# Kernel tuning notes

Hardware: AMD Instinct MI355X
Metric: run time of the kernel (lower is better)

Reference implementation:

```python
import jax, jax.numpy as jnp
import numpy as np

N_NODES = 50000
N_EDGES = 800000
FEAT_IN = 128
POS_IN = 16
EDGE_FEAT_IN = 16
H = 64
L = 4


def _lin(k, fan_in, fan_out):
    kw, kb = jax.random.split(k)
    s = 1.0 / np.sqrt(fan_in)
    W = jax.random.uniform(kw, (fan_in, fan_out), minval=-s, maxval=s, dtype=jnp.float32)
    b = jax.random.uniform(kb, (fan_out,), minval=-s, maxval=s, dtype=jnp.float32)
    return W, b


def setup_inputs() -> dict:
    key = jax.random.key(0)
    ks = jax.random.split(key, 32)
    h = jax.random.normal(ks[0], (N_NODES, FEAT_IN), dtype=jnp.float32)
    e = jax.random.normal(ks[1], (N_EDGES, EDGE_FEAT_IN), dtype=jnp.float32)
    p = jax.random.normal(ks[2], (N_NODES, POS_IN), dtype=jnp.float32)
    edge_index = jax.random.randint(ks[3], (2, N_EDGES), 0, N_NODES, dtype=jnp.int64 if jax.config.x64_enabled else jnp.int32)
    he_W, he_b = _lin(ks[4], FEAT_IN, H)
    ee_W, ee_b = _lin(ks[5], EDGE_FEAT_IN, H)
    pe_W, pe_b = _lin(ks[6], POS_IN, H)

    def stack(fan_in, base):
        Ws, bs = [], []
        for i in range(L):
            W, b = _lin(jax.random.fold_in(ks[7], base * 100 + i), fan_in, H)
            Ws.append(W); bs.append(b)
        return jnp.stack(Ws), jnp.stack(bs)

    hm_W, hm_b = stack(5 * H, 0)  # h_message_mlp
    hu_W, hu_b = stack(2 * H, 1)  # h_update
    eu_W, eu_b = stack(3 * H, 2)  # e_update
    pm_W, pm_b = stack(3 * H, 3)  # p_message_mlp
    pu_W, pu_b = stack(2 * H, 4)  # p_update
    return dict(h=h, e=e, p=p, edge_index=edge_index,
                he_W=he_W, he_b=he_b, ee_W=ee_W, ee_b=ee_b, pe_W=pe_W, pe_b=pe_b,
                hm_W=hm_W, hm_b=hm_b, hu_W=hu_W, hu_b=hu_b,
                eu_W=eu_W, eu_b=eu_b, pm_W=pm_W, pm_b=pm_b, pu_W=pu_W, pu_b=pu_b)


def reference(h, e, p, edge_index, he_W, he_b, ee_W, ee_b, pe_W, pe_b,
              hm_W, hm_b, hu_W, hu_b, eu_W, eu_b, pm_W, pm_b, pu_W, pu_b):
    send, rec = edge_index[0], edge_index[1]
    n = h.shape[0]
    h = h @ he_W + he_b  # [N,H]
    e = e @ ee_W + ee_b  # [E,H]
    p = p @ pe_W + pe_b  # [N,H]
    for i in range(L):
        hp_send = jnp.concatenate((h[send], p[send]), axis=1)  # [E,2H]
        hp_rec = jnp.concatenate((h[rec], p[rec]), axis=1)     # [E,2H]
        h_msg = jnp.concatenate((hp_send, hp_rec, e), axis=1) @ hm_W[i] + hm_b[i]  # [E,H]
        h_agg = jax.ops.segment_sum(h_msg, rec, num_segments=n)  # [N,H]
        h = jnp.concatenate((h, h_agg), axis=1) @ hu_W[i] + hu_b[i]
        e = jnp.concatenate((h[send], h[rec], e), axis=1) @ eu_W[i] + eu_b[i]
        p_msg = jnp.concatenate((p[send], p[rec], e), axis=1) @ pm_W[i] + pm_b[i]
        p_agg = jax.ops.segment_sum(p_msg, rec, num_segments=n)
        p = jnp.concatenate((p, p_agg), axis=1) @ pu_W[i] + pu_b[i]
    return (h, p)
```

## Files before the change

### kernel.cpp

```cpp
#include <hip/hip_runtime.h>
#include <hip/hip_bf16.h>

#define NN 50000
#define NE 800000

typedef __hip_bfloat16 bf16;
typedef __attribute__((ext_vector_type(8))) short bf16x8s;
typedef __attribute__((ext_vector_type(4))) float f32x4;

#define OFF_HP     0L
#define OFF_HSUM   12800000L
#define OFF_PSUM   25600000L
#define OFF_ESUM   38400000L
#define OFF_EAGGA  41600000L
#define OFF_EAGGB  54400000L
#define OFF_WFMT   67200000L
#define OFF_ROWPTR 67716096L
#define OFF_COLIDX 67916100L
#define OFF_SSEND  71116100L
#define OFF_SEG    74316100L
#define OFF_CNT    77516100L
#define OFF_BSUM   77716100L

#define SCAN_B 196

#define FW_HE 0
#define FW_EE 8192
#define FW_PE 10240
#define FW_L0 12288
#define LSTR  61440
#define R_HAGG 0
#define R_HMR  12288
#define R_HU   20480
#define R_EUS  28672
#define R_EUR  32768
#define R_EUE  36864
#define R_PAGG 40960
#define R_PMR  49152
#define R_PU   53248

#define AGG_STRIDE 72

__device__ __forceinline__ bf16x8s bfrag(const bf16* w, int c, int t, int lane) {
    return *(const bf16x8s*)(w + ((long)(c*4 + t)*64 + lane)*8);
}
__device__ __forceinline__ bf16x8s cvt8(const float* fp) {
    float4 f0 = ((const float4*)fp)[0];
    float4 f1 = ((const float4*)fp)[1];
    bf16 tmp[8];
    tmp[0]=__float2bfloat16(f0.x); tmp[1]=__float2bfloat16(f0.y);
    tmp[2]=__float2bfloat16(f0.z); tmp[3]=__float2bfloat16(f0.w);
    tmp[4]=__float2bfloat16(f1.x); tmp[5]=__float2bfloat16(f1.y);
    tmp[6]=__float2bfloat16(f1.z); tmp[7]=__float2bfloat16(f1.w);
    return *(const bf16x8s*)tmp;
}

__global__ __launch_bounds__(256) void wfmt_k(
    const float* __restrict__ he, const float* __restrict__ ee, const float* __restrict__ pe,
    const float* __restrict__ hm, const float* __restrict__ hu, const float* __restrict__ eu,
    const float* __restrict__ pm, const float* __restrict__ pu, bf16* __restrict__ wf)
{
    int s = blockIdx.x;
    const float* src = nullptr; int rowoff = 0, Ksrc = 0, Kpad = 0, mode = 0, split = 0, gap = 0; long doff = 0;
    if      (s == 0) { src = he; Ksrc = 128; Kpad = 128; doff = FW_HE; }
    else if (s == 1) { src = ee; Ksrc = 16;  Kpad = 32;  doff = FW_EE; }
    else if (s == 2) { src = pe; Ksrc = 16;  Kpad = 32;  doff = FW_PE; }
    else {
        int i = (s - 3) / 9, g = (s - 3) % 9;
        long base = FW_L0 + (long)i*LSTR;
        const float* HM = hm + (long)i*320*64;
        const float* HU = hu + (long)i*128*64;
        const float* EU = eu + (long)i*192*64;
        const float* PM = pm + (long)i*192*64;
        const float* PU = pu + (long)i*128*64;
        switch (g) {
          case 0:  src=HM; mode=4; split=128; gap=128; Kpad=192; doff=base+R_HAGG; break;
          case 1:  src=HM; rowoff=128; Ksrc=128; Kpad=128; doff=base+R_HMR;  break;
          case 2:  src=HU; rowoff=0;   Ksrc=128; Kpad=128; doff=base+R_HU;   break;
          case 3:  src=EU; rowoff=0;   Ksrc=64;  Kpad=64;  doff=base+R_EUS;  break;
          case 4:  src=EU; rowoff=64;  Ksrc=64;  Kpad=64;  doff=base+R_EUR;  break;
          case 5:  src=EU; rowoff=128; Ksrc=64;  Kpad=64;  doff=base+R_EUE;  break;
          case 6:  src=PM; mode=4; split=64; gap=64; Kpad=128; doff=base+R_PAGG; break;
          case 7:  src=PM; rowoff=64;  Ksrc=64;  Kpad=64;  doff=base+R_PMR;  break;
          default: src=PU; rowoff=0;   Ksrc=128; Kpad=128; doff=base+R_PU;   break;
        }
    }
    int total = Kpad * 64;
    for (int idx = threadIdx.x; idx < total; idx += 256) {
        int j = idx & 7, l = (idx >> 3) & 63, ct = idx >> 9;
        int c = ct >> 2, t = ct & 3;
        int k = c*32 + (l >> 4)*8 + j;
        int n = t*16 + (l & 15);
        float v;
        if (mode == 4) v = src[(long)(k + (k >= split ? gap : 0))*64 + n];
        else           v = (k < Ksrc) ? src[(long)(rowoff + k)*64 + n] : 0.f;
        wf[doff + idx] = __float2bfloat16(v);
    }
}

__global__ __launch_bounds__(256) void hist_k(const int* __restrict__ rec, int* __restrict__ cnt)
{
    int e = blockIdx.x*256 + threadIdx.x;
    if (e < NE) atomicAdd(&cnt[rec[e]], 1);
}

__global__ __launch_bounds__(256) void scan1_k(const int* __restrict__ cnt, int* __restrict__ bsum)
{
    __shared__ int sdata[256];
    int tid = threadIdx.x;
    int i = blockIdx.x*256 + tid;
    sdata[tid] = (i < NN) ? cnt[i] : 0;
    __syncthreads();
    #pragma unroll
    for (int off = 128; off > 0; off >>= 1) {
        if (tid < off) sdata[tid] += sdata[tid + off];
        __syncthreads();
    }
    if (tid == 0) bsum[blockIdx.x] = sdata[0];
}

__global__ __launch_bounds__(256) void scan2_k(int* __restrict__ bsum)
{
    __shared__ int sdata[256];
    int tid = threadIdx.x;
    int v = (tid < SCAN_B) ? bsum[tid] : 0;
    sdata[tid] = v;
    __syncthreads();
    #pragma unroll
    for (int off = 1; off < 256; off <<= 1) {
        int t = (tid >= off) ? sdata[tid - off] : 0;
        __syncthreads();
        sdata[tid] += t;
        __syncthreads();
    }
    if (tid < SCAN_B) bsum[tid] = sdata[tid] - v;
}

__global__ __launch_bounds__(256) void scan3_k(const int* __restrict__ cnt,
    const int* __restrict__ bsum, int* __restrict__ rowptr)
{
    __shared__ int sdata[256];
    int tid = threadIdx.x;
    int i = blockIdx.x*256 + tid;
    sdata[tid] = (i < NN) ? cnt[i] : 0;
    __syncthreads();
    #pragma unroll
    for (int off = 1; off < 256; off <<= 1) {
        int t = (tid >= off) ? sdata[tid - off] : 0;
        __syncthreads();
        sdata[tid] += t;
        __syncthreads();
    }
    if (i < NN) rowptr[i + 1] = sdata[tid] + bsum[blockIdx.x];
    if (i == 0) rowptr[0] = 0;
}

__global__ __launch_bounds__(256) void scatter_k(const int* __restrict__ rec,
    const int* __restrict__ rowptr, int* __restrict__ cursor, int* __restrict__ colidx)
{
    int e = blockIdx.x*256 + threadIdx.x;
    if (e < NE) {
        int r = rec[e];
        int pos = atomicAdd(&cursor[r], 1);
        colidx[rowptr[r] + pos] = e;
    }
}

__global__ __launch_bounds__(256) void segfill_k(const int* __restrict__ rowptr, int* __restrict__ seg)
{
    int n = blockIdx.x*256 + threadIdx.x;
    if (n < NN) {
        int b = rowptr[n], e = rowptr[n + 1];
        for (int j = b; j < e; ++j) seg[j] = n;
    }
}

template <int DEPTH, bool BOTH>
__global__ __launch_bounds__(256) void gsum64_k(const bf16* __restrict__ hp, int coff,
    const int* __restrict__ ssend, const int* __restrict__ seg,
    float* __restrict__ out1, float* __restrict__ out2)
{
    __shared__ int s_ids[256];
    __shared__ int s_seg[256];
    int tid = threadIdx.x, lane = tid & 63, wv = tid >> 6;
    int gbase = blockIdx.x*256;
    s_ids[tid] = ssend[gbase + tid];
    s_seg[tid] = seg[gbase + tid];
    __syncthreads();
    int j0 = wv*64;
    const bf16* base = hp + coff + lane;
    constexpr int NB = 64 / DEPTH;

    unsigned short va[DEPTH], vb[DEPTH];
    unsigned short wa[BOTH ? DEPTH : 1], wb[BOTH ? DEPTH : 1];
    #pragma unroll
    for (int k = 0; k < DEPTH; ++k) {
        long o = (long)s_ids[j0 + k]*128;
        va[k] = *(const unsigned short*)(base + o);
        if (BOTH) wa[k] = *(const unsigned short*)(base + o + 64);
    }

    float a = 0.f, b2 = 0.f;
    int cur = s_seg[j0];
    #pragma unroll
    for (int b = 0; b < NB; ++b) {
        if (b < NB - 1) {
            #pragma unroll
            for (int k = 0; k < DEPTH; ++k) {
                long o = (long)s_ids[j0 + (b+1)*DEPTH + k]*128;
                vb[k] = *(const unsigned short*)(base + o);
                if (BOTH) wb[k] = *(const unsigned short*)(base + o + 64);
            }
        }
        #pragma unroll
        for (int k = 0; k < DEPTH; ++k) {
            int n = s_seg[j0 + b*DEPTH + k];
            if (n != cur) {
                atomicAdd(&out1[(long)cur*64 + lane], a);
                if (BOTH) atomicAdd(&out2[(long)cur*64 + lane], b2);
                a = 0.f; b2 = 0.f; cur = n;
            }
            a += __uint_as_float(((unsigned)va[k]) << 16);
            if (BOTH) b2 += __uint_as_float(((unsigned)wa[k]) << 16);
        }
        if (b < NB - 1) {
            #pragma unroll
            for (int k = 0; k < DEPTH; ++k) { va[k] = vb[k]; if (BOTH) wa[k] = wb[k]; }
        }
    }
    atomicAdd(&out1[(long)cur*64 + lane], a);
    if (BOTH) atomicAdd(&out2[(long)cur*64 + lane], b2);
}

__global__ __launch_bounds__(256) void esum_k(const float* __restrict__ e_in,
    const int* __restrict__ colidx, const int* __restrict__ seg, const int* __restrict__ send,
    int* __restrict__ ssend, float* __restrict__ esum)
{
    __shared__ int s_ids[256];
    __shared__ int s_seg[256];
    int tid = threadIdx.x;
    int gbase = blockIdx.x*256;
    int id = colidx[gbase + tid];
    s_ids[tid] = id;
    s_seg[tid] = seg[gbase + tid];
    ssend[gbase + tid] = send[id];
    __syncthreads();
    int grp = tid >> 4, c = tid & 15;
    int j0 = grp*16;
    float vv[16];
    #pragma unroll
    for (int jj = 0; jj < 16; ++jj) vv[jj] = e_in[(long)s_ids[j0 + jj]*16 + c];
    float a = 0.f;
    int cur = s_seg[j0];
    #pragma unroll
    for (int jj = 0; jj < 16; ++jj) {
        int n = s_seg[j0 + jj];
        if (n != cur) { atomicAdd(&esum[(long)cur*16 + c], a); a = 0.f; cur = n; }
        a += vv[jj];
    }
    atomicAdd(&esum[(long)cur*16 + c], a);
}

__global__ __launch_bounds__(256) void eembn_k(const float* __restrict__ esum,
    const int* __restrict__ deg, const bf16* __restrict__ wEE, const float* __restrict__ ee_b,
    bf16* __restrict__ eagg)
{
    int tid = threadIdx.x, lane = tid & 63, wv = tid >> 6;
    int l15 = lane & 15, q = lane >> 4;
    int row = blockIdx.x*64 + wv*16 + l15;
    int rc = (row < NN) ? row : NN - 1;
    f32x4 acc[4];
    #pragma unroll
    for (int t = 0; t < 4; ++t) { acc[t][0]=0; acc[t][1]=0; acc[t][2]=0; acc[t][3]=0; }
    {
        bf16x8s af = {0,0,0,0,0,0,0,0};
        if (q < 2) af = cvt8(esum + (long)rc*16 + q*8);
        #pragma unroll
        for (int t = 0; t < 4; ++t)
            acc[t] = __builtin_amdgcn_mfma_f32_16x16x32_bf16(af, bfrag(wEE, 0, t, lane), acc[t], 0, 0, 0);
    }
    float bv[4];
    #pragma unroll
    for (int t = 0; t < 4; ++t) bv[t] = ee_b[t*16 + l15];
    #pragma unroll
    for (int r = 0; r < 4; ++r) {
        int ro = blockIdx.x*64 + wv*16 + q*4 + r;
        if (ro < NN) {
            float dg = (float)deg[ro];
            #pragma unroll
            for (int t = 0; t < 4; ++t)
                eagg[(long)ro*64 + t*16 + l15] = __float2bfloat16(acc[t][r] + dg*bv[t]);
        }
    }
}

__global__ __launch_bounds__(256) void hpemb_k(const float* __restrict__ h_in,
    const float* __restrict__ p_in,
    const bf16* __restrict__ wHE, const bf16* __restrict__ wPE,
    const float* __restrict__ he_b, const float* __restrict__ pe_b, bf16* __restrict__ hp)
{
    int tid = threadIdx.x, lane = tid & 63, wv = tid >> 6;
    int l15 = lane & 15, q = lane >> 4;
    int row = blockIdx.x*64 + wv*16 + l15;
    int rc = (row < NN) ? row : NN - 1;
    f32x4 aH[4], aP[4];
    #pragma unroll
    for (int t = 0; t < 4; ++t) {
        float bh = he_b[t*16 + l15], bp = pe_b[t*16 + l15];
        aH[t][0]=bh; aH[t][1]=bh; aH[t][2]=bh; aH[t][3]=bh;
        aP[t][0]=bp; aP[t][1]=bp; aP[t][2]=bp; aP[t][3]=bp;
    }
    #pragma unroll
    for (int c = 0; c < 4; ++c) {
        bf16x8s af = cvt8(h_in + (long)rc*128 + c*32 + q*8);
        #pragma unroll
        for (int t = 0; t < 4; ++t)
            aH[t] = __builtin_amdgcn_mfma_f32_16x16x32_bf16(af, bfrag(wHE, c, t, lane), aH[t], 0, 0, 0);
    }
    {
        bf16x8s af = {0,0,0,0,0,0,0,0};
        if (q < 2) af = cvt8(p_in + (long)rc*16 + q*8);
        #pragma unroll
        for (int t = 0; t < 4; ++t)
            aP[t] = __builtin_amdgcn_mfma_f32_16x16x32_bf16(af, bfrag(wPE, 0, t, lane), aP[t], 0, 0, 0);
    }
    #pragma unroll
    for (int r = 0; r < 4; ++r) {
        int ro = blockIdx.x*64 + wv*16 + q*4 + r;
        if (ro < NN)
            #pragma unroll
            for (int t = 0; t < 4; ++t) {
                hp[(long)ro*128 + t*16 + l15]      = __float2bfloat16(aH[t][r]);
                hp[(long)ro*128 + 64 + t*16 + l15] = __float2bfloat16(aP[t][r]);
            }
    }
}

__global__ __launch_bounds__(256) void hfuse_k(
    bf16* __restrict__ hp, float* __restrict__ hsum, const float* __restrict__ psum,
    const bf16* __restrict__ eagg, const int* __restrict__ deg,
    const bf16* __restrict__ wAGG, const bf16* __restrict__ wR, const float* __restrict__ mb,
    const bf16* __restrict__ wU, const float* __restrict__ ub, float* __restrict__ out2)
{
    __shared__ __align__(16) bf16 sAgg[64 * AGG_STRIDE];
    int tid = threadIdx.x, lane = tid & 63, wv = tid >> 6;
    int l15 = lane & 15, q = lane >> 4;
    int row = blockIdx.x*64 + wv*16 + l15;
    int rc = (row < NN) ? row : NN - 1;

    f32x4 aA[4], aR[4];
    #pragma unroll
    for (int t = 0; t < 4; ++t) {
        aA[t][0]=0;aA[t][1]=0;aA[t][2]=0;aA[t][3]=0;
        aR[t][0]=0;aR[t][1]=0;aR[t][2]=0;aR[t][3]=0;
    }
    #pragma unroll
    for (int c = 0; c < 6; ++c) {
        bf16x8s af = (c < 2) ? cvt8(hsum + (long)rc*64 + c*32 + q*8)
                   : (c < 4) ? cvt8(psum + (long)rc*64 + (c-2)*32 + q*8)
                             : *(const bf16x8s*)(eagg + (long)rc*64 + (c-4)*32 + q*8);
        #pragma unroll
        for (int t = 0; t < 4; ++t)
            aA[t] = __builtin_amdgcn_mfma_f32_16x16x32_bf16(af, bfrag(wAGG, c, t, lane), aA[t], 0, 0, 0);
    }
    if (row < NN) {
        float4 z4 = make_float4(0.f, 0.f, 0.f, 0.f);
        #pragma unroll
        for (int c = 0; c < 2; ++c) {
            *(float4*)(hsum + (long)rc*64 + c*32 + q*8)     = z4;
            *(float4*)(hsum + (long)rc*64 + c*32 + q*8 + 4) = z4;
        }
    }
    #pragma unroll
    for (int c = 0; c < 4; ++c) {
        bf16x8s af = *(const bf16x8s*)(hp + (long)rc*128 + c*32 + q*8);
        #pragma unroll
        for (int t = 0; t < 4; ++t)
            aR[t] = __builtin_amdgcn_mfma_f32_16x16x32_bf16(af, bfrag(wR, c, t, lane), aR[t], 0, 0, 0);
    }
    float mbv[4];
    #pragma unroll
    for (int t = 0; t < 4; ++t) mbv[t] = mb[t*16 + l15];
    #pragma unroll
    for (int r = 0; r < 4; ++r) {
        int ro = blockIdx.x*64 + wv*16 + q*4 + r;
        float dg = (float)deg[(ro < NN) ? ro : NN - 1];
        #pragma unroll
        for (int t = 0; t < 4; ++t)
            sAgg[(wv*16 + q*4 + r)*AGG_STRIDE + t*16 + l15] =
                __float2bfloat16(aA[t][r] + dg*(aR[t][r] + mbv[t]));
    }
    __syncthreads();
    f32x4 acc[4];
    #pragma unroll
    for (int t = 0; t < 4; ++t) { float b = ub[t*16 + l15]; acc[t][0]=b; acc[t][1]=b; acc[t][2]=b; acc[t][3]=b; }
    #pragma unroll
    for (int c = 0; c < 4; ++c) {
        bf16x8s af = (c < 2) ? *(const bf16x8s*)(hp + (long)rc*128 + c*32 + q*8)
                             : *(const bf16x8s*)(sAgg + (wv*16 + l15)*AGG_STRIDE + (c-2)*32 + q*8);
        #pragma unroll
        for (int t = 0; t < 4; ++t)
            acc[t] = __builtin_amdgcn_mfma_f32_16x16x32_bf16(af, bfrag(wU, c, t, lane), acc[t], 0, 0, 0);
    }
    #pragma unroll
    for (int r = 0; r < 4; ++r) {
        int ro = blockIdx.x*64 + wv*16 + q*4 + r;
        if (ro < NN) {
            #pragma unroll
            for (int t = 0; t < 4; ++t) {
                float fv = acc[t][r];
                hp[(long)ro*128 + t*16 + l15] = __float2bfloat16(fv);
                if (out2) out2[(long)ro*64 + t*16 + l15] = fv;
            }
        }
    }
}

__global__ __launch_bounds__(256) void pfuse_k(
    bf16* __restrict__ hp, const float* __restrict__ hsumN, float* __restrict__ psum,
    const bf16* __restrict__ eaggIn, bf16* __restrict__ eaggOut, const int* __restrict__ deg,
    const bf16* __restrict__ wEUS, const bf16* __restrict__ wEUR, const bf16* __restrict__ wEUE,
    const float* __restrict__ eub,
    const bf16* __restrict__ wAGG, const bf16* __restrict__ wR, const float* __restrict__ mb,
    const bf16* __restrict__ wU, const float* __restrict__ ub, float* __restrict__ out2)
{
    __shared__ __align__(16) bf16 sE[64 * AGG_STRIDE];
    __shared__ __align__(16) bf16 sAgg[64 * AGG_STRIDE];
    int tid = threadIdx.x, lane = tid & 63, wv = tid >> 6;
    int l15 = lane & 15, q = lane >> 4;
    int row = blockIdx.x*64 + wv*16 + l15;
    int rc = (row < NN) ? row : NN - 1;

    f32x4 aE[4], aH[4];
    #pragma unroll
    for (int t = 0; t < 4; ++t) {
        aE[t][0]=0;aE[t][1]=0;aE[t][2]=0;aE[t][3]=0;
        aH[t][0]=0;aH[t][1]=0;aH[t][2]=0;aH[t][3]=0;
    }
    #pragma unroll
    for (int c = 0; c < 4; ++c) {
        bf16x8s af = (c < 2) ? cvt8(hsumN + (long)rc*64 + c*32 + q*8)
                             : *(const bf16x8s*)(eaggIn + (long)rc*64 + (c-2)*32 + q*8);
        #pragma unroll
        for (int t = 0; t < 4; ++t) {
            bf16x8s w = (c < 2) ? bfrag(wEUS, c, t, lane) : bfrag(wEUE, c-2, t, lane);
            aE[t] = __builtin_amdgcn_mfma_f32_16x16x32_bf16(af, w, aE[t], 0, 0, 0);
        }
    }
    #pragma unroll
    for (int c = 0; c < 2; ++c) {
        bf16x8s af = *(const bf16x8s*)(hp + (long)rc*128 + c*32 + q*8);
        #pragma unroll
        for (int t = 0; t < 4; ++t)
            aH[t] = __builtin_amdgcn_mfma_f32_16x16x32_bf16(af, bfrag(wEUR, c, t, lane), aH[t], 0, 0, 0);
    }
    float ebv[4];
    #pragma unroll
    for (int t = 0; t < 4; ++t) ebv[t] = eub[t*16 + l15];
    #pragma unroll
    for (int r = 0; r < 4; ++r) {
        int ro = blockIdx.x*64 + wv*16 + q*4 + r;
        float dg = (float)deg[(ro < NN) ? ro : NN - 1];
        #pragma unroll
        for (int t = 0; t < 4; ++t) {
            bf16 ev = __float2bfloat16(aE[t][r] + dg*(aH[t][r] + ebv[t]));
            sE[(wv*16 + q*4 + r)*AGG_STRIDE + t*16 + l15] = ev;
            if (eaggOut && ro < NN) eaggOut[(long)ro*64 + t*16 + l15] = ev;
        }
    }
    __syncthreads();

    f32x4 aA[4], aR[4];
    #pragma unroll
    for (int t = 0; t < 4; ++t) {
        aA[t][0]=0;aA[t][1]=0;aA[t][2]=0;aA[t][3]=0;
        aR[t][0]=0;aR[t][1]=0;aR[t][2]=0;aR[t][3]=0;
    }
    #pragma unroll
    for (int c = 0; c < 4; ++c) {
        bf16x8s af = (c < 2) ? cvt8(psum + (long)rc*64 + c*32 + q*8)
                             : *(const bf16x8s*)(sE + (wv*16 + l15)*AGG_STRIDE + (c-2)*32 + q*8);
        #pragma unroll
        for (int t = 0; t < 4; ++t)
            aA[t] = __builtin_amdgcn_mfma_f32_16x16x32_bf16(af, bfrag(wAGG, c, t, lane), aA[t], 0, 0, 0);
    }
    if (row < NN) {
        float4 z4 = make_float4(0.f, 0.f, 0.f, 0.f);
        #pragma unroll
        for (int c = 0; c < 2; ++c) {
            *(float4*)(psum + (long)rc*64 + c*32 + q*8)     = z4;
            *(float4*)(psum + (long)rc*64 + c*32 + q*8 + 4) = z4;
        }
    }
    #pragma unroll
    for (int c = 0; c < 2; ++c) {
        bf16x8s af = *(const bf16x8s*)(hp + (long)rc*128 + 64 + c*32 + q*8);
        #pragma unroll
        for (int t = 0; t < 4; ++t)
            aR[t] = __builtin_amdgcn_mfma_f32_16x16x32_bf16(af, bfrag(wR, c, t, lane), aR[t], 0, 0, 0);
    }
    float mbv[4];
    #pragma unroll
    for (int t = 0; t < 4; ++t) mbv[t] = mb[t*16 + l15];
    #pragma unroll
    for (int r = 0; r < 4; ++r) {
        int ro = blockIdx.x*64 + wv*16 + q*4 + r;
        float dg = (float)deg[(ro < NN) ? ro : NN - 1];
        #pragma unroll
        for (int t = 0; t < 4; ++t)
            sAgg[(wv*16 + q*4 + r)*AGG_STRIDE + t*16 + l15] =
                __float2bfloat16(aA[t][r] + dg*(aR[t][r] + mbv[t]));
    }
    __syncthreads();
    f32x4 acc[4];
    #pragma unroll
    for (int t = 0; t < 4; ++t) { float b = ub[t*16 + l15]; acc[t][0]=b; acc[t][1]=b; acc[t][2]=b; acc[t][3]=b; }
    #pragma unroll
    for (int c = 0; c < 4; ++c) {
        bf16x8s af = (c < 2) ? *(const bf16x8s*)(hp + (long)rc*128 + 64 + c*32 + q*8)
                             : *(const bf16x8s*)(sAgg + (wv*16 + l15)*AGG_STRIDE + (c-2)*32 + q*8);
        #pragma unroll
        for (int t = 0; t < 4; ++t)
            acc[t] = __builtin_amdgcn_mfma_f32_16x16x32_bf16(af, bfrag(wU, c, t, lane), acc[t], 0, 0, 0);
    }
    #pragma unroll
    for (int r = 0; r < 4; ++r) {
        int ro = blockIdx.x*64 + wv*16 + q*4 + r;
        if (ro < NN) {
            #pragma unroll
            for (int t = 0; t < 4; ++t) {
                float fv = acc[t][r];
                hp[(long)ro*128 + 64 + t*16 + l15] = __float2bfloat16(fv);
                if (out2) out2[(long)ro*64 + t*16 + l15] = fv;
            }
        }
    }
}

extern "C" void kernel_launch(void* const* d_in, const int* in_sizes, int n_in,
                              void* d_out, int out_size, void* d_ws, size_t ws_size,
                              hipStream_t stream)
{
    (void)in_sizes; (void)n_in; (void)out_size; (void)ws_size;
    const float* h_in = (const float*)d_in[0];
    const float* e_in = (const float*)d_in[1];
    const float* p_in = (const float*)d_in[2];
    const int*  ei   = (const int*)d_in[3];
    const int* send = ei;
    const int* rec  = ei + NE;
    const float* he_W = (const float*)d_in[4];  const float* he_b = (const float*)d_in[5];
    const float* ee_W = (const float*)d_in[6];  const float* ee_b = (const float*)d_in[7];
    const float* pe_W = (const float*)d_in[8];  const float* pe_b = (const float*)d_in[9];
    const float* hm_W = (const float*)d_in[10]; const float* hm_b = (const float*)d_in[11];
    const float* hu_W = (const float*)d_in[12]; const float* hu_b = (const float*)d_in[13];
    const float* eu_W = (const float*)d_in[14]; const float* eu_b = (const float*)d_in[15];
    const float* pm_W = (const float*)d_in[16]; const float* pm_b = (const float*)d_in[17];
    const float* pu_W = (const float*)d_in[18]; const float* pu_b = (const float*)d_in[19];

    char* ws = (char*)d_ws;
    bf16* hp     = (bf16*)(ws + OFF_HP);
    float* hsum  = (float*)(ws + OFF_HSUM);
    float* psum  = (float*)(ws + OFF_PSUM);
    float* esum  = (float*)(ws + OFF_ESUM);
    bf16* eaggA  = (bf16*)(ws + OFF_EAGGA);
    bf16* eaggB  = (bf16*)(ws + OFF_EAGGB);
    bf16* wf     = (bf16*)(ws + OFF_WFMT);
    int* rowptr  = (int*)(ws + OFF_ROWPTR);
    int* colidx  = (int*)(ws + OFF_COLIDX);
    int* ssend   = (int*)(ws + OFF_SSEND);
    int* segarr  = (int*)(ws + OFF_SEG);
    int* cnt     = (int*)(ws + OFF_CNT);
    int* bsum    = (int*)(ws + OFF_BSUM);
    float* dout  = (float*)d_out;

    const int EB   = NE / 256;
    const int NB64 = (NN + 63) / 64;

    (void)hipMemsetAsync(cnt, 0, NN * sizeof(int), stream);
    hist_k<<<EB, 256, 0, stream>>>(rec, cnt);
    scan1_k<<<SCAN_B, 256, 0, stream>>>(cnt, bsum);
    scan2_k<<<1, 256, 0, stream>>>(bsum);
    scan3_k<<<SCAN_B, 256, 0, stream>>>(cnt, bsum, rowptr);
    (void)hipMemsetAsync(cnt, 0, NN * sizeof(int), stream);
    scatter_k<<<EB, 256, 0, stream>>>(rec, rowptr, cnt, colidx);
    segfill_k<<<SCAN_B, 256, 0, stream>>>(rowptr, segarr);

    (void)hipMemsetAsync(hsum, 0, (long)NN*(64 + 64 + 16)*sizeof(float), stream);

    esum_k<<<EB, 256, 0, stream>>>(e_in, colidx, segarr, send, ssend, esum);

    wfmt_k<<<39, 256, 0, stream>>>(he_W, ee_W, pe_W, hm_W, hu_W, eu_W, pm_W, pu_W, wf);

    hpemb_k<<<NB64, 256, 0, stream>>>(h_in, p_in, wf + FW_HE, wf + FW_PE, he_b, pe_b, hp);
    eembn_k<<<NB64, 256, 0, stream>>>(esum, cnt, wf + FW_EE, ee_b, eaggA);
    gsum64_k<16, true><<<EB, 256, 0, stream>>>(hp, 0, ssend, segarr, hsum, psum);

    bf16* eA = eaggA;
    bf16* eB = eaggB;
    for (int i = 0; i < 4; ++i) {
        long base = FW_L0 + (long)i*LSTR;
        hfuse_k<<<NB64, 256, 0, stream>>>(hp, hsum, psum, eA, cnt,
            wf + base + R_HAGG, wf + base + R_HMR, hm_b + i*64,
            wf + base + R_HU, hu_b + i*64,
            (i == 3) ? dout : nullptr);
        gsum64_k<32, false><<<EB, 256, 0, stream>>>(hp, 0, ssend, segarr, hsum, nullptr);
        pfuse_k<<<NB64, 256, 0, stream>>>(hp, hsum, psum, eA, (i < 3) ? eB : nullptr, cnt,
            wf + base + R_EUS, wf + base + R_EUR, wf + base + R_EUE, eu_b + i*64,
            wf + base + R_PAGG, wf + base + R_PMR, pm_b + i*64,
            wf + base + R_PU, pu_b + i*64,
            (i == 3) ? dout + (long)NN*64 : nullptr);
        if (i < 3)
            gsum64_k<32, false><<<EB, 256, 0, stream>>>(hp, 64, ssend, segarr, psum, nullptr);
        bf16* tmp = eA; eA = eB; eB = tmp;
    }
}
```

Baseline: 657.3 us.

## Fuse main GNN pipeline into one persistent cooperative kernel with grid syncs

Replaces the chain of per-layer kernel launches (embedding, gather-sums, h/p fused updates) with a single cooperative persistent kernel. Blocks loop over tiles and use grid.sync between stages, falling back to separate launches when cooperative launch is unavailable. It also merges the edge-embedding kernel into the node-embedding kernel and folds segfill into scan3. The aim is to cut launch gaps and tail effects, at the cost of grid-sync overhead, reduced occupancy from shared smem and register pressure, and the gsum stage losing its deeper DEPTH=32 prefetch.

```diff
diff --git a/kernel.cpp b/kernel.cpp
--- a/kernel.cpp
+++ b/kernel.cpp
@@ -1,8 +1,12 @@
 #include <hip/hip_runtime.h>
 #include <hip/hip_bf16.h>
+#include <hip/hip_cooperative_groups.h>
+namespace cg = cooperative_groups;
 
 #define NN 50000
 #define NE 800000
+#define NB64 782
+#define EB   3125
 
 typedef __hip_bfloat16 bf16;
 typedef __attribute__((ext_vector_type(8))) short bf16x8s;
@@ -137,12 +141,13 @@
 }
 
 __global__ __launch_bounds__(256) void scan3_k(const int* __restrict__ cnt,
-    const int* __restrict__ bsum, int* __restrict__ rowptr)
+    const int* __restrict__ bsum, int* __restrict__ rowptr, int* __restrict__ seg)
 {
     __shared__ int sdata[256];
     int tid = threadIdx.x;
     int i = blockIdx.x*256 + tid;
-    sdata[tid] = (i < NN) ? cnt[i] : 0;
+    int v = (i < NN) ? cnt[i] : 0;
+    sdata[tid] = v;
     __syncthreads();
     #pragma unroll
     for (int off = 1; off < 256; off <<= 1) {
@@ -151,7 +156,11 @@
         sdata[tid] += t;
         __syncthreads();
     }
-    if (i < NN) rowptr[i + 1] = sdata[tid] + bsum[blockIdx.x];
+    if (i < NN) {
+        int hi = sdata[tid] + bsum[blockIdx.x];
+        rowptr[i + 1] = hi;
+        for (int j = hi - v; j < hi; ++j) seg[j] = i;
+    }
     if (i == 0) rowptr[0] = 0;
 }
 
@@ -164,72 +173,6 @@
         int pos = atomicAdd(&cursor[r], 1);
         colidx[rowptr[r] + pos] = e;
     }
-}
-
-__global__ __launch_bounds__(256) void segfill_k(const int* __restrict__ rowptr, int* __restrict__ seg)
-{
-    int n = blockIdx.x*256 + threadIdx.x;
-    if (n < NN) {
-        int b = rowptr[n], e = rowptr[n + 1];
-        for (int j = b; j < e; ++j) seg[j] = n;
-    }
-}
-
-template <int DEPTH, bool BOTH>
-__global__ __launch_bounds__(256) void gsum64_k(const bf16* __restrict__ hp, int coff,
-    const int* __restrict__ ssend, const int* __restrict__ seg,
-    float* __restrict__ out1, float* __restrict__ out2)
-{
-    __shared__ int s_ids[256];
-    __shared__ int s_seg[256];
-    int tid = threadIdx.x, lane = tid & 63, wv = tid >> 6;
-    int gbase = blockIdx.x*256;
-    s_ids[tid] = ssend[gbase + tid];
-    s_seg[tid] = seg[gbase + tid];
-    __syncthreads();
-    int j0 = wv*64;
-    const bf16* base = hp + coff + lane;
-    constexpr int NB = 64 / DEPTH;
-
-    unsigned short va[DEPTH], vb[DEPTH];
-    unsigned short wa[BOTH ? DEPTH : 1], wb[BOTH ? DEPTH : 1];
-    #pragma unroll
-    for (int k = 0; k < DEPTH; ++k) {
-        long o = (long)s_ids[j0 + k]*128;
-        va[k] = *(const unsigned short*)(base + o);
-        if (BOTH) wa[k] = *(const unsigned short*)(base + o + 64);
-    }
-
-    float a = 0.f, b2 = 0.f;
-    int cur = s_seg[j0];
-    #pragma unroll
-    for (int b = 0; b < NB; ++b) {
-        if (b < NB - 1) {
-            #pragma unroll
-            for (int k = 0; k < DEPTH; ++k) {
-                long o = (long)s_ids[j0 + (b+1)*DEPTH + k]*128;
-                vb[k] = *(const unsigned short*)(base + o);
-                if (BOTH) wb[k] = *(const unsigned short*)(base + o + 64);
-            }
-        }
-        #pragma unroll
-        for (int k = 0; k < DEPTH; ++k) {
-            int n = s_seg[j0 + b*DEPTH + k];
-            if (n != cur) {
-                atomicAdd(&out1[(long)cur*64 + lane], a);
-                if (BOTH) atomicAdd(&out2[(long)cur*64 + lane], b2);
-                a = 0.f; b2 = 0.f; cur = n;
-            }
-            a += __uint_as_float(((unsigned)va[k]) << 16);
-            if (BOTH) b2 += __uint_as_float(((unsigned)wa[k]) << 16);
-        }
-        if (b < NB - 1) {
-            #pragma unroll
-            for (int k = 0; k < DEPTH; ++k) { va[k] = vb[k]; if (BOTH) wa[k] = wb[k]; }
-        }
-    }
-    atomicAdd(&out1[(long)cur*64 + lane], a);
-    if (BOTH) atomicAdd(&out2[(long)cur*64 + lane], b2);
 }
 
 __global__ __launch_bounds__(256) void esum_k(const float* __restrict__ e_in,
@@ -261,54 +204,79 @@
     atomicAdd(&esum[(long)cur*16 + c], a);
 }
 
-__global__ __launch_bounds__(256) void eembn_k(const float* __restrict__ esum,
-    const int* __restrict__ deg, const bf16* __restrict__ wEE, const float* __restrict__ ee_b,
-    bf16* __restrict__ eagg)
+
+template <bool BOTH>
+__device__ __forceinline__ void gsum_body(const bf16* __restrict__ hp, int coff,
+    const int* __restrict__ ssend, const int* __restrict__ seg,
+    float* __restrict__ out1, float* __restrict__ out2,
+    int gbase, int* s_ids, int* s_seg)
+{
+    int tid = threadIdx.x, lane = tid & 63, wv = tid >> 6;
+    s_ids[tid] = ssend[gbase + tid];
+    s_seg[tid] = seg[gbase + tid];
+    __syncthreads();
+    int j0 = wv*64;
+    const bf16* base = hp + coff + lane;
+
+    unsigned short va[16], vb[16];
+    unsigned short wa[BOTH ? 16 : 1], wb[BOTH ? 16 : 1];
+    #pragma unroll
+    for (int k = 0; k < 16; ++k) {
+        long o = (long)s_ids[j0 + k]*128;
+        va[k] = *(const unsigned short*)(base + o);
+        if (BOTH) wa[k] = *(const unsigned short*)(base + o + 64);
+    }
+    float a = 0.f, b2 = 0.f;
+    int cur = s_seg[j0];
+    #pragma unroll
+    for (int b = 0; b < 4; ++b) {
+        if (b < 3) {
+            #pragma unroll
+            for (int k = 0; k < 16; ++k) {
+                long o = (long)s_ids[j0 + (b+1)*16 + k]*128;
+                vb[k] = *(const unsigned short*)(base + o);
+                if (BOTH) wb[k] = *(const unsigned short*)(base + o + 64);
+            }
+        }
+        #pragma unroll
+        for (int k = 0; k < 16; ++k) {
+            int n = s_seg[j0 + b*16 + k];
+            if (n != cur) {
+                atomicAdd(&out1[(long)cur*64 + lane], a);
+                if (BOTH) atomicAdd(&out2[(long)cur*64 + lane], b2);
+                a = 0.f; b2 = 0.f; cur = n;
+            }
+            a += __uint_as_float(((unsigned)va[k]) << 16);
+            if (BOTH) b2 += __uint_as_float(((unsigned)wa[k]) << 16);
+        }
+        if (b < 3) {
+            #pragma unroll
+            for (int k = 0; k < 16; ++k) { va[k] = vb[k]; if (BOTH) wa[k] = wb[k]; }
+        }
+    }
+    atomicAdd(&out1[(long)cur*64 + lane], a);
+    if (BOTH) atomicAdd(&out2[(long)cur*64 + lane], b2);
+    __syncthreads();
+}
+
+__device__ __forceinline__ void hpemb_body(int blk,
+    const float* __restrict__ h_in, const float* __restrict__ p_in,
+    const float* __restrict__ esum, const int* __restrict__ deg,
+    const bf16* __restrict__ wHE, const bf16* __restrict__ wPE, const bf16* __restrict__ wEE,
+    const float* __restrict__ he_b, const float* __restrict__ pe_b, const float* __restrict__ ee_b,
+    bf16* __restrict__ hp, bf16* __restrict__ eagg)
 {
     int tid = threadIdx.x, lane = tid & 63, wv = tid >> 6;
     int l15 = lane & 15, q = lane >> 4;
-    int row = blockIdx.x*64 + wv*16 + l15;
+    int row = blk*64 + wv*16 + l15;
     int rc = (row < NN) ? row : NN - 1;
-    f32x4 acc[4];
-    #pragma unroll
-    for (int t = 0; t < 4; ++t) { acc[t][0]=0; acc[t][1]=0; acc[t][2]=0; acc[t][3]=0; }
-    {
-        bf16x8s af = {0,0,0,0,0,0,0,0};
-        if (q < 2) af = cvt8(esum + (long)rc*16 + q*8);
-        #pragma unroll
-        for (int t = 0; t < 4; ++t)
-            acc[t] = __builtin_amdgcn_mfma_f32_16x16x32_bf16(af, bfrag(wEE, 0, t, lane), acc[t], 0, 0, 0);
-    }
-    float bv[4];
-    #pragma unroll
-    for (int t = 0; t < 4; ++t) bv[t] = ee_b[t*16 + l15];
-    #pragma unroll
-    for (int r = 0; r < 4; ++r) {
-        int ro = blockIdx.x*64 + wv*16 + q*4 + r;
-        if (ro < NN) {
-            float dg = (float)deg[ro];
-            #pragma unroll
-            for (int t = 0; t < 4; ++t)
-                eagg[(long)ro*64 + t*16 + l15] = __float2bfloat16(acc[t][r] + dg*bv[t]);
-        }
-    }
-}
-
-__global__ __launch_bounds__(256) void hpemb_k(const float* __restrict__ h_in,
-    const float* __restrict__ p_in,
-    const bf16* __restrict__ wHE, const bf16* __restrict__ wPE,
-    const float* __restrict__ he_b, const float* __restrict__ pe_b, bf16* __restrict__ hp)
-{
-    int tid = threadIdx.x, lane = tid & 63, wv = tid >> 6;
-    int l15 = lane & 15, q = lane >> 4;
-    int row = blockIdx.x*64 + wv*16 + l15;
-    int rc = (row < NN) ? row : NN - 1;
-    f32x4 aH[4], aP[4];
+    f32x4 aH[4], aP[4], aE[4];
     #pragma unroll
     for (int t = 0; t < 4; ++t) {
         float bh = he_b[t*16 + l15], bp = pe_b[t*16 + l15];
         aH[t][0]=bh; aH[t][1]=bh; aH[t][2]=bh; aH[t][3]=bh;
         aP[t][0]=bp; aP[t][1]=bp; aP[t][2]=bp; aP[t][3]=bp;
+        aE[t][0]=0;  aE[t][1]=0;  aE[t][2]=0;  aE[t][3]=0;
     }
     #pragma unroll
     for (int c = 0; c < 4; ++c) {
@@ -324,28 +292,41 @@
         for (int t = 0; t < 4; ++t)
             aP[t] = __builtin_amdgcn_mfma_f32_16x16x32_bf16(af, bfrag(wPE, 0, t, lane), aP[t], 0, 0, 0);
     }
+    {
+        bf16x8s af = {0,0,0,0,0,0,0,0};
+        if (q < 2) af = cvt8(esum + (long)rc*16 + q*8);
+        #pragma unroll
+        for (int t = 0; t < 4; ++t)
+            aE[t] = __builtin_amdgcn_mfma_f32_16x16x32_bf16(af, bfrag(wEE, 0, t, lane), aE[t], 0, 0, 0);
+    }
+    float ebv[4];
+    #pragma unroll
+    for (int t = 0; t < 4; ++t) ebv[t] = ee_b[t*16 + l15];
     #pragma unroll
     for (int r = 0; r < 4; ++r) {
-        int ro = blockIdx.x*64 + wv*16 + q*4 + r;
-        if (ro < NN)
+        int ro = blk*64 + wv*16 + q*4 + r;
+        if (ro < NN) {
+            float dg = (float)deg[ro];
             #pragma unroll
             for (int t = 0; t < 4; ++t) {
                 hp[(long)ro*128 + t*16 + l15]      = __float2bfloat16(aH[t][r]);
                 hp[(long)ro*128 + 64 + t*16 + l15] = __float2bfloat16(aP[t][r]);
+                eagg[(long)ro*64 + t*16 + l15]     = __float2bfloat16(aE[t][r] + dg*ebv[t]);
             }
-    }
-}
-
-__global__ __launch_bounds__(256) void hfuse_k(
+        }
+    }
+}
+
+__device__ __forceinline__ void hfuse_body(int blk,
     bf16* __restrict__ hp, float* __restrict__ hsum, const float* __restrict__ psum,
     const bf16* __restrict__ eagg, const int* __restrict__ deg,
     const bf16* __restrict__ wAGG, const bf16* __restrict__ wR, const float* __restrict__ mb,
-    const bf16* __restrict__ wU, const float* __restrict__ ub, float* __restrict__ out2)
-{
-    __shared__ __align__(16) bf16 sAgg[64 * AGG_STRIDE];
+    const bf16* __restrict__ wU, const float* __restrict__ ub, float* __restrict__ out2,
+    bf16* sAgg)
+{
     int tid = threadIdx.x, lane = tid & 63, wv = tid >> 6;
     int l15 = lane & 15, q = lane >> 4;
-    int row = blockIdx.x*64 + wv*16 + l15;
+    int row = blk*64 + wv*16 + l15;
     int rc = (row < NN) ? row : NN - 1;
 
     f32x4 aA[4], aR[4];
@@ -383,7 +364,7 @@
     for (int t = 0; t < 4; ++t) mbv[t] = mb[t*16 + l15];
     #pragma unroll
     for (int r = 0; r < 4; ++r) {
-        int ro = blockIdx.x*64 + wv*16 + q*4 + r;
+        int ro = blk*64 + wv*16 + q*4 + r;
         float dg = (float)deg[(ro < NN) ? ro : NN - 1];
         #pragma unroll
         for (int t = 0; t < 4; ++t)
@@ -404,7 +385,7 @@
     }
     #pragma unroll
     for (int r = 0; r < 4; ++r) {
-        int ro = blockIdx.x*64 + wv*16 + q*4 + r;
+        int ro = blk*64 + wv*16 + q*4 + r;
         if (ro < NN) {
             #pragma unroll
             for (int t = 0; t < 4; ++t) {
@@ -414,21 +395,21 @@
             }
         }
     }
-}
-
-__global__ __launch_bounds__(256) void pfuse_k(
+    __syncthreads();
+}
+
+__device__ __forceinline__ void pfuse_body(int blk,
     bf16* __restrict__ hp, const float* __restrict__ hsumN, float* __restrict__ psum,
     const bf16* __restrict__ eaggIn, bf16* __restrict__ eaggOut, const int* __restrict__ deg,
     const bf16* __restrict__ wEUS, const bf16* __restrict__ wEUR, const bf16* __restrict__ wEUE,
     const float* __restrict__ eub,
     const bf16* __restrict__ wAGG, const bf16* __restrict__ wR, const float* __restrict__ mb,
-    const bf16* __restrict__ wU, const float* __restrict__ ub, float* __restrict__ out2)
-{
-    __shared__ __align__(16) bf16 sE[64 * AGG_STRIDE];
-    __shared__ __align__(16) bf16 sAgg[64 * AGG_STRIDE];
+    const bf16* __restrict__ wU, const float* __restrict__ ub, float* __restrict__ out2,
+    bf16* sE, bf16* sAgg)
+{
     int tid = threadIdx.x, lane = tid & 63, wv = tid >> 6;
     int l15 = lane & 15, q = lane >> 4;
-    int row = blockIdx.x*64 + wv*16 + l15;
+    int row = blk*64 + wv*16 + l15;
     int rc = (row < NN) ? row : NN - 1;
 
     f32x4 aE[4], aH[4];
@@ -459,7 +440,7 @@
     for (int t = 0; t < 4; ++t) ebv[t] = eub[t*16 + l15];
     #pragma unroll
     for (int r = 0; r < 4; ++r) {
-        int ro = blockIdx.x*64 + wv*16 + q*4 + r;
+        int ro = blk*64 + wv*16 + q*4 + r;
         float dg = (float)deg[(ro < NN) ? ro : NN - 1];
         #pragma unroll
         for (int t = 0; t < 4; ++t) {
@@ -504,7 +485,7 @@
     for (int t = 0; t < 4; ++t) mbv[t] = mb[t*16 + l15];
     #pragma unroll
     for (int r = 0; r < 4; ++r) {
-        int ro = blockIdx.x*64 + wv*16 + q*4 + r;
+        int ro = blk*64 + wv*16 + q*4 + r;
         float dg = (float)deg[(ro < NN) ? ro : NN - 1];
         #pragma unroll
         for (int t = 0; t < 4; ++t)
@@ -525,7 +506,7 @@
     }
     #pragma unroll
     for (int r = 0; r < 4; ++r) {
-        int ro = blockIdx.x*64 + wv*16 + q*4 + r;
+        int ro = blk*64 + wv*16 + q*4 + r;
         if (ro < NN) {
             #pragma unroll
             for (int t = 0; t < 4; ++t) {
@@ -534,6 +515,101 @@
                 if (out2) out2[(long)ro*64 + t*16 + l15] = fv;
             }
         }
+    }
+    __syncthreads();
+}
+
+__global__ __launch_bounds__(256) void hpemb_k(const float* h_in, const float* p_in,
+    const float* esum, const int* deg, const bf16* wHE, const bf16* wPE, const bf16* wEE,
+    const float* he_b, const float* pe_b, const float* ee_b, bf16* hp, bf16* eagg)
+{
+    hpemb_body(blockIdx.x, h_in, p_in, esum, deg, wHE, wPE, wEE, he_b, pe_b, ee_b, hp, eagg);
+}
+
+template <bool BOTH>
+__global__ __launch_bounds__(256) void gsum64_k(const bf16* hp, int coff,
+    const int* ssend, const int* seg, float* out1, float* out2)
+{
+    __shared__ int s_ids[256];
+    __shared__ int s_seg[256];
+    gsum_body<BOTH>(hp, coff, ssend, seg, out1, out2, blockIdx.x*256, s_ids, s_seg);
+}
+
+__global__ __launch_bounds__(256) void hfuse_k(bf16* hp, float* hsum, const float* psum,
+    const bf16* eagg, const int* deg, const bf16* wAGG, const bf16* wR, const float* mb,
+    const bf16* wU, const float* ub, float* out2)
+{
+    __shared__ __align__(16) bf16 sAgg[64 * AGG_STRIDE];
+    hfuse_body(blockIdx.x, hp, hsum, psum, eagg, deg, wAGG, wR, mb, wU, ub, out2, sAgg);
+}
+
+__global__ __launch_bounds__(256) void pfuse_k(bf16* hp, const float* hsumN, float* psum,
+    const bf16* eaggIn, bf16* eaggOut, const int* deg,
+    const bf16* wEUS, const bf16* wEUR, const bf16* wEUE, const float* eub,
+    const bf16* wAGG, const bf16* wR, const float* mb,
+    const bf16* wU, const float* ub, float* out2)
+{
+    __shared__ __align__(16) bf16 sE[64 * AGG_STRIDE];
+    __shared__ __align__(16) bf16 sAgg[64 * AGG_STRIDE];
+    pfuse_body(blockIdx.x, hp, hsumN, psum, eaggIn, eaggOut, deg, wEUS, wEUR, wEUE, eub,
+               wAGG, wR, mb, wU, ub, out2, sE, sAgg);
+}
+
+struct MegaArgs {
+    const float* h_in; const float* p_in; const float* esum;
+    bf16* hp; float* hsum; float* psum; bf16* eaggA; bf16* eaggB;
+    const int* ssend; const int* seg; const int* deg;
+    const bf16* wf;
+    const float* he_b; const float* pe_b; const float* ee_b;
+    const float* hm_b; const float* hu_b; const float* eu_b;
+    const float* pm_b; const float* pu_b;
+    float* dout;
+};
+
+__global__ __launch_bounds__(256) void mega_k(MegaArgs a)
+{
+    __shared__ __align__(16) bf16 smem[2 * 64 * AGG_STRIDE];
+    int* s_ids = (int*)smem;
+    int* s_seg = ((int*)smem) + 256;
+    bf16* sE   = smem;
+    bf16* sAgg = smem + 64 * AGG_STRIDE;
+    cg::grid_group grid = cg::this_grid();
+    int G = gridDim.x;
+
+    for (int t = blockIdx.x; t < NB64; t += G)
+        hpemb_body(t, a.h_in, a.p_in, a.esum, a.deg,
+                   a.wf + FW_HE, a.wf + FW_PE, a.wf + FW_EE,
+                   a.he_b, a.pe_b, a.ee_b, a.hp, a.eaggA);
+    grid.sync();
+    for (int t = blockIdx.x; t < EB; t += G)
+        gsum_body<true>(a.hp, 0, a.ssend, a.seg, a.hsum, a.psum, t*256, s_ids, s_seg);
+    grid.sync();
+
+    bf16* eA = a.eaggA;
+    bf16* eB = a.eaggB;
+    for (int i = 0; i < 4; ++i) {
+        const bf16* base = a.wf + FW_L0 + (long)i*LSTR;
+        for (int t = blockIdx.x; t < NB64; t += G)
+            hfuse_body(t, a.hp, a.hsum, a.psum, eA, a.deg,
+                       base + R_HAGG, base + R_HMR, a.hm_b + i*64,
+                       base + R_HU, a.hu_b + i*64, (i == 3) ? a.dout : nullptr, sAgg);
+        grid.sync();
+        for (int t = blockIdx.x; t < EB; t += G)
+            gsum_body<false>(a.hp, 0, a.ssend, a.seg, a.hsum, nullptr, t*256, s_ids, s_seg);
+        grid.sync();
+        for (int t = blockIdx.x; t < NB64; t += G)
+            pfuse_body(t, a.hp, a.hsum, a.psum, eA, (i < 3) ? eB : nullptr, a.deg,
+                       base + R_EUS, base + R_EUR, base + R_EUE, a.eu_b + i*64,
+                       base + R_PAGG, base + R_PMR, a.pm_b + i*64,
+                       base + R_PU, a.pu_b + i*64,
+                       (i == 3) ? a.dout + (long)NN*64 : nullptr, sE, sAgg);
+        grid.sync();
+        if (i < 3) {
+            for (int t = blockIdx.x; t < EB; t += G)
+                gsum_body<false>(a.hp, 64, a.ssend, a.seg, a.psum, nullptr, t*256, s_ids, s_seg);
+            grid.sync();
+        }
+        bf16* tmp = eA; eA = eB; eB = tmp;
     }
 }
 
@@ -573,44 +649,68 @@
     int* bsum    = (int*)(ws + OFF_BSUM);
     float* dout  = (float*)d_out;
 
-    const int EB   = NE / 256;
-    const int NB64 = (NN + 63) / 64;
+    static int g_grid = -1;
+    if (g_grid < 0) {
+        hipDeviceProp_t prop;
+        if (hipGetDeviceProperties(&prop, 0) == hipSuccess && prop.cooperativeLaunch) {
+            int bpcu = 0;
+            if (hipOccupancyMaxActiveBlocksPerMultiprocessor(&bpcu, mega_k, 256, 0) == hipSuccess
+                && bpcu >= 1) {
+                long g = (long)bpcu * prop.multiProcessorCount;
+                g_grid = (int)((g > EB) ? EB : g);
+            } else g_grid = 0;
+        } else g_grid = 0;
+    }
 
     (void)hipMemsetAsync(cnt, 0, NN * sizeof(int), stream);
     hist_k<<<EB, 256, 0, stream>>>(rec, cnt);
     scan1_k<<<SCAN_B, 256, 0, stream>>>(cnt, bsum);
     scan2_k<<<1, 256, 0, stream>>>(bsum);
-    scan3_k<<<SCAN_B, 256, 0, stream>>>(cnt, bsum, rowptr);
+    scan3_k<<<SCAN_B, 256, 0, stream>>>(cnt, bsum, rowptr, segarr);
     (void)hipMemsetAsync(cnt, 0, NN * sizeof(int), stream);
     scatter_k<<<EB, 256, 0, stream>>>(rec, rowptr, cnt, colidx);
-    segfill_k<<<SCAN_B, 256, 0, stream>>>(rowptr, segarr);
 
     (void)hipMemsetAsync(hsum, 0, (long)NN*(64 + 64 + 16)*sizeof(float), stream);
 
     esum_k<<<EB, 256, 0, stream>>>(e_in, colidx, segarr, send, ssend, esum);
-
     wfmt_k<<<39, 256, 0, stream>>>(he_W, ee_W, pe_W, hm_W, hu_W, eu_W, pm_W, pu_W, wf);
 
-    hpemb_k<<<NB64, 256, 0, stream>>>(h_in, p_in, wf + FW_HE, wf + FW_PE, he_b, pe_b, hp);
-    eembn_k<<<NB64, 256, 0, stream>>>(esum, cnt, wf + FW_EE, ee_b, eaggA);
-    gsum64_k<16, true><<<EB, 256, 0, stream>>>(hp, 0, ssend, segarr, hsum, psum);
-
-    bf16* eA = eaggA;
-    bf16* eB = eaggB;
-    for (int i = 0; i < 4; ++i) {
-        long base = FW_L0 + (long)i*LSTR;
-        hfuse_k<<<NB64, 256, 0, stream>>>(hp, hsum, psum, eA, cnt,
-            wf + base + R_HAGG, wf + base + R_HMR, hm_b + i*64,
-            wf + base + R_HU, hu_b + i*64,
-            (i == 3) ? dout : nullptr);
-        gsum64_k<32, false><<<EB, 256, 0, stream>>>(hp, 0, ssend, segarr, hsum, nullptr);
-        pfuse_k<<<NB64, 256, 0, stream>>>(hp, hsum, psum, eA, (i < 3) ? eB : nullptr, cnt,
-            wf + base + R_EUS, wf + base + R_EUR, wf + base + R_EUE, eu_b + i*64,
-            wf + base + R_PAGG, wf + base + R_PMR, pm_b + i*64,
-            wf + base + R_PU, pu_b + i*64,
-            (i == 3) ? dout + (long)NN*64 : nullptr);
-        if (i < 3)
-            gsum64_k<32, false><<<EB, 256, 0, stream>>>(hp, 64, ssend, segarr, psum, nullptr);
-        bf16* tmp = eA; eA = eB; eB = tmp;
-    }
-}
+    bool coop_done = false;
+    if (g_grid > 0) {
+        MegaArgs ma;
+        ma.h_in = h_in; ma.p_in = p_in; ma.esum = esum;
+        ma.hp = hp; ma.hsum = hsum; ma.psum = psum; ma.eaggA = eaggA; ma.eaggB = eaggB;
+        ma.ssend = ssend; ma.seg = segarr; ma.deg = cnt; ma.wf = wf;
+        ma.he_b = he_b; ma.pe_b = pe_b; ma.ee_b = ee_b;
+        ma.hm_b = hm_b; ma.hu_b = hu_b; ma.eu_b = eu_b; ma.pm_b = pm_b; ma.pu_b = pu_b;
+        ma.dout = dout;
+        void* params[] = { &ma };
+        hipError_t err = hipLaunchCooperativeKernel((const void*)mega_k,
+            dim3(g_grid), dim3(256), params, 0, stream);
+        if (err == hipSuccess) coop_done = true;
+        else g_grid = 0;
+    }
+
+    if (!coop_done) {
+        hpemb_k<<<NB64, 256, 0, stream>>>(h_in, p_in, esum, cnt,
+            wf + FW_HE, wf + FW_PE, wf + FW_EE, he_b, pe_b, ee_b, hp, eaggA);
+        gsum64_k<true><<<EB, 256, 0, stream>>>(hp, 0, ssend, segarr, hsum, psum);
+        bf16* eA = eaggA;
+        bf16* eB = eaggB;
+        for (int i = 0; i < 4; ++i) {
+            long base = FW_L0 + (long)i*LSTR;
+            hfuse_k<<<NB64, 256, 0, stream>>>(hp, hsum, psum, eA, cnt,
+                wf + base + R_HAGG, wf + base + R_HMR, hm_b + i*64,
+                wf + base + R_HU, hu_b + i*64, (i == 3) ? dout : nullptr);
+            gsum64_k<false><<<EB, 256, 0, stream>>>(hp, 0, ssend, segarr, hsum, nullptr);
+            pfuse_k<<<NB64, 256, 0, stream>>>(hp, hsum, psum, eA, (i < 3) ? eB : nullptr, cnt,
+                wf + base + R_EUS, wf + base + R_EUR, wf + base + R_EUE, eu_b + i*64,
+                wf + base + R_PAGG, wf + base + R_PMR, pm_b + i*64,
+                wf + base + R_PU, pu_b + i*64,
+                (i == 3) ? dout + (long)NN*64 : nullptr);
+            if (i < 3)
+                gsum64_k<false><<<EB, 256, 0, stream>>>(hp, 64, ssend, segarr, psum, nullptr);
+            bf16* tmp = eA; eA = eB; eB = tmp;
+        }
+    }
+}
```

Measured after the change: 622.3 us. 5.3% less time.
